# Optimization experiments

Measured on AMD Instinct MI355X. Metric: run time of the kernel, lower is better.

## Reference

```python
import jax, jax.numpy as jnp
import numpy as np

SHADOW_OFFSET = -1000.0
EPS_SIGMA = 1e-05
SIGMA_DIV = 2.1


def setup_inputs() -> dict:
    key = jax.random.key(0)
    k1, k2, k3, k4, k5, k6 = jax.random.split(key, 6)
    B, N, M, K, Kp, Din, Dout = 2, 65536, 16384, 32, 15, 64, 128
    points_xyz = jax.random.normal(k1, (B, N, 3), dtype=jnp.float32)
    features = jax.random.normal(k2, (B, Din, N), dtype=jnp.float32)
    center_xyz = jax.random.normal(k3, (B, M, 3), dtype=jnp.float32)
    neighbor_indices = jax.random.randint(k4, (B, M, K), 0, N + 1, dtype=jnp.int64)
    # kernel points in unit ball, 'center' fixed at origin (stand-in for load_kernels)
    kp = jax.random.normal(k5, (Kp, 3), dtype=jnp.float32)
    kp = kp / (jnp.linalg.norm(kp, axis=-1, keepdims=True) + 1e-6) * jax.random.uniform(k6, (Kp, 1)) ** (1.0 / 3.0)
    kernel_points = kp.at[0].set(0.0)
    # kaiming_uniform(a=sqrt(5)) on [Kp, Din, Dout]: fan_in = Din*Dout per torch semantics
    fan_in = Din * Dout
    bound = jnp.sqrt(6.0 / ((1.0 + 5.0) * fan_in)) * jnp.sqrt(3.0) / jnp.sqrt(3.0)
    bound = float(np.sqrt(6.0 / (6.0 * fan_in)))
    weights = jax.random.uniform(jax.random.fold_in(key, 7), (Kp, Din, Dout), minval=-bound, maxval=bound, dtype=jnp.float32)
    return {"points_xyz": points_xyz, "features": features, "center_xyz": center_xyz,
            "neighbor_indices": neighbor_indices, "kernel_points": kernel_points, "weights": weights}


def reference(points_xyz, features, center_xyz, neighbor_indices, kernel_points, weights):
    B, N, _ = points_xyz.shape
    M, K = neighbor_indices.shape[1], neighbor_indices.shape[2]
    Din = features.shape[1]
    # [B,N,3+Din] point coords + features, plus shadow point at index N
    points = jnp.concatenate([points_xyz, jnp.swapaxes(features, 1, 2)], axis=-1)
    shadow = jnp.zeros((B, 1, 3 + Din), points.dtype).at[:, :, :3].set(SHADOW_OFFSET)
    points = jnp.concatenate([points, shadow], axis=1)  # [B,N+1,3+Din]
    idx = neighbor_indices.reshape(B, M * K)
    gathered = jnp.take_along_axis(points, idx[:, :, None], axis=1).reshape(B, M, K, 3 + Din)
    neighbors_xyz = gathered[..., :3] - center_xyz[:, :, None, :]   # [B,M,K,3]
    neighbors_feats = gathered[..., 3:]                              # [B,M,K,Din]
    dist = jnp.sqrt(jnp.sum(neighbors_xyz ** 2, axis=3))             # [B,M,K]
    m_dist = jnp.max(dist, axis=2, keepdims=True)                    # [B,M,1]
    # radius=None path: kernel points scaled per center by max neighbor distance
    kp = kernel_points[None, None, :, :] * m_dist[:, :, :, None]     # [B,M,Kp,3]
    diffs = neighbors_xyz[:, :, :, None, :] - kp[:, :, None, :, :]   # [B,M,K,Kp,3]
    sq_d = jnp.sum(diffs ** 2, axis=4)                               # [B,M,K,Kp]
    sigma = m_dist[..., None] / SIGMA_DIV + EPS_SIGMA                # [B,M,1,1]
    w = jnp.clip(1.0 - jnp.sqrt(sq_d) / sigma, 0.0)                  # [B,M,K,Kp]
    weighted = jnp.einsum('bmkp,bmkd->bmpd', w, neighbors_feats)     # [B,M,Kp,Din]
    out = jnp.einsum('bmpd,pdo->bmo', weighted, weights)             # [B,M,Dout]
    return jnp.swapaxes(out, 1, 2)                                   # [B,Dout,M]
```

## Files before the change

kernel.cpp:

```cpp
#include <hip/hip_runtime.h>
#include <hip/hip_bf16.h>
#include <stdint.h>

#define B_    2
#define N_    65536
#define M_    16384
#define K_    32
#define KP_   15
#define DIN_  64
#define DOUT_ 128
#define TM    16
#define WPITCH 968

typedef __bf16 bf16x8 __attribute__((ext_vector_type(8)));
typedef float  f32x4  __attribute__((ext_vector_type(4)));
typedef float  f32x2  __attribute__((ext_vector_type(2)));

__device__ inline unsigned short f2bf(float f) {
    union { float f; unsigned int i; } v; v.f = f;
    unsigned int x = v.i;
    return (unsigned short)((x + 0x7fffu + ((x >> 16) & 1u)) >> 16);
}

__global__ __launch_bounds__(256) void transpose_feats(const float* __restrict__ feats,
                                                       unsigned short* __restrict__ featT) {
    const int b  = blockIdx.y;
    const int n0 = blockIdx.x * 64;
    const int t  = threadIdx.x;
    if (n0 >= N_) {
        if (t < 32)
            ((unsigned int*)(featT + ((size_t)b * (N_ + 1) + N_) * DIN_))[t] = 0u;
        return;
    }
    __shared__ float tile[64][65];
    const int nl = t & 63, dl = t >> 6;
    #pragma unroll
    for (int i = 0; i < 16; ++i) {
        int d = dl + 4 * i;
        tile[d][nl] = feats[((size_t)b * DIN_ + d) * N_ + n0 + nl];
    }
    __syncthreads();
    const int d2 = (t & 31) * 2;
    const int nr = t >> 5;
    #pragma unroll
    for (int i = 0; i < 8; ++i) {
        int n = nr + 8 * i;
        unsigned int u = ((unsigned int)f2bf(tile[d2 + 1][n]) << 16) | f2bf(tile[d2][n]);
        ((unsigned int*)(featT + ((size_t)b * (N_ + 1) + n0 + n) * DIN_))[t & 31] = u;
    }
}

__global__ __launch_bounds__(256) void build_wtfrag(const float* __restrict__ w,
                                                    unsigned short* __restrict__ wf) {
    int q = blockIdx.x * 256 + threadIdx.x;
    if (q >= 15360) return;
    int otile = q / 1920, r = q % 1920;
    int ks = r >> 6, lane = r & 63;
    int o  = otile * 16 + (lane & 15);
    int kb = ks * 32 + (lane >> 4) * 8;
    unsigned int d[4];
    #pragma unroll
    for (int j = 0; j < 4; ++j) {
        unsigned short lo = f2bf(w[(size_t)(kb + 2 * j) * 128 + o]);
        unsigned short hi = f2bf(w[(size_t)(kb + 2 * j + 1) * 128 + o]);
        d[j] = ((unsigned int)hi << 16) | lo;
    }
    *(uint4*)(wf + (size_t)q * 8) = make_uint4(d[0], d[1], d[2], d[3]);
}

__global__ __launch_bounds__(512, 1) void kpconv_fused(
    const float* __restrict__ points_xyz,
    const float* __restrict__ center_xyz,
    const int*   __restrict__ nidx,
    const float* __restrict__ kpts,
    const unsigned short* __restrict__ featT,
    const unsigned short* __restrict__ wtFrag,
    float* __restrict__ out) {

    __shared__ __align__(16) unsigned int  fbuf[TM * 32 * 32];
    __shared__ __align__(16) float         wlds[TM * KP_ * 32];
    __shared__ __align__(16) unsigned short wgt[TM * WPITCH];

    const int t  = threadIdx.x;
    const int b  = blockIdx.y;
    const int m0 = blockIdx.x * TM;
    const size_t ibase = ((size_t)b * M_ + m0) * K_;

    uint4 v[8];
    const int part = t & 7, rbase = t >> 3;
    #pragma unroll
    for (int i = 0; i < 8; ++i) {
        int r = i * 64 + rbase;
        int n = nidx[ibase + r];
        v[i] = *(const uint4*)(featT + ((size_t)b * (N_ + 1) + n) * DIN_ + part * 8);
    }

    {
        const int m = t >> 5, k = t & 31;
        int n = nidx[ibase + t];
        float px, py, pz;
        if (n < N_) {
            const float* p = points_xyz + ((size_t)b * N_ + n) * 3;
            px = p[0]; py = p[1]; pz = p[2];
        } else {
            px = py = pz = -1000.0f;
        }
        const float* c = center_xyz + ((size_t)b * M_ + m0 + m) * 3;
        float dx = px - c[0], dy = py - c[1], dz = pz - c[2];
        float md = __builtin_amdgcn_sqrtf(dx * dx + dy * dy + dz * dz);
        #pragma unroll
        for (int s = 16; s > 0; s >>= 1)
            md = fmaxf(md, __shfl_xor(md, s));
        float rsig = __builtin_amdgcn_rcpf(md * (1.0f / 2.1f) + 1e-5f);
        #pragma unroll
        for (int p = 0; p < KP_; ++p) {
            float ex = dx - kpts[p * 3 + 0] * md;
            float ey = dy - kpts[p * 3 + 1] * md;
            float ez = dz - kpts[p * 3 + 2] * md;
            float wv = 1.0f - __builtin_amdgcn_sqrtf(ex * ex + ey * ey + ez * ez) * rsig;
            wlds[(m * KP_ + p) * 32 + k] = wv > 0.0f ? wv : 0.0f;
        }
    }

    #pragma unroll
    for (int i = 0; i < 8; ++i)
        ((uint4*)fbuf)[(i * 64 + rbase) * 8 + part] = v[i];
    __syncthreads();

    {
        const int m = t >> 5, d2 = t & 31;
        f32x2 acc[KP_];
        #pragma unroll
        for (int p = 0; p < KP_; ++p) acc[p] = (f32x2){0.f, 0.f};

        const unsigned int* fcol = &fbuf[(m * 32) * 32 + d2];
        const float* wbase = &wlds[m * KP_ * 32];

        #pragma unroll
        for (int k4 = 0; k4 < 8; ++k4) {
            f32x2 fv[4];
            #pragma unroll
            for (int j = 0; j < 4; ++j) {
                unsigned int u = fcol[(k4 * 4 + j) * 32];
                union { unsigned int i; float f; } lo, hi;
                lo.i = u << 16; hi.i = u & 0xffff0000u;
                fv[j] = (f32x2){lo.f, hi.f};
            }
            #pragma unroll
            for (int p = 0; p < KP_; ++p) {
                float4 w4 = *(const float4*)(wbase + p * 32 + k4 * 4);
                acc[p] += fv[0] * w4.x;
                acc[p] += fv[1] * w4.y;
                acc[p] += fv[2] * w4.z;
                acc[p] += fv[3] * w4.w;
            }
        }

        unsigned int* wrow = (unsigned int*)wgt;
        #pragma unroll
        for (int p = 0; p < KP_; ++p) {
            unsigned int u = ((unsigned int)f2bf(acc[p][1]) << 16) | f2bf(acc[p][0]);
            wrow[m * (WPITCH / 2) + p * 32 + d2] = u;
        }
    }
    __syncthreads();

    {
        const int w = t >> 6, lane = t & 63;
        const char* aBase = (const char*)wgt + (lane & 15) * (WPITCH * 2) + (lane >> 4) * 16;
        const unsigned short* bPtr = wtFrag + ((size_t)(w * 30) * 64 + lane) * 8;

        f32x4 dacc = {0.f, 0.f, 0.f, 0.f};
        bf16x8 b0 = *(const bf16x8*)(bPtr);
        bf16x8 b1 = *(const bf16x8*)(bPtr + 512);
        bf16x8 b2 = *(const bf16x8*)(bPtr + 1024);
        bf16x8 b3 = *(const bf16x8*)(bPtr + 1536);
        bf16x8 b4 = *(const bf16x8*)(bPtr + 2048);

        #define S2_STEP(BX, KS, LD)                                           \
            {                                                                 \
                bf16x8 a = *(const bf16x8*)(aBase + (KS) * 64);               \
                dacc = __builtin_amdgcn_mfma_f32_16x16x32_bf16(a, BX, dacc,   \
                                                               0, 0, 0);      \
                if ((LD) < 30) BX = *(const bf16x8*)(bPtr + (size_t)(LD) * 512); \
            }

        for (int mi = 0; mi < 6; ++mi) {
            int ks = mi * 5;
            S2_STEP(b0, ks + 0, ks + 5);
            S2_STEP(b1, ks + 1, ks + 6);
            S2_STEP(b2, ks + 2, ks + 7);
            S2_STEP(b3, ks + 3, ks + 8);
            S2_STEP(b4, ks + 4, ks + 9);
        }
        #undef S2_STEP

        const int o = w * 16 + (lane & 15);
        float* dst = out + ((size_t)b * DOUT_ + o) * M_ + m0 + (lane >> 4) * 4;
        *(f32x4*)dst = dacc;
    }
}

extern "C" void kernel_launch(void* const* d_in, const int* in_sizes, int n_in,
                              void* d_out, int out_size, void* d_ws, size_t ws_size,
                              hipStream_t stream) {
    const float* points_xyz = (const float*)d_in[0];
    const float* features   = (const float*)d_in[1];
    const float* center_xyz = (const float*)d_in[2];
    const int*   nidx       = (const int*)d_in[3];
    const float* kpts       = (const float*)d_in[4];
    const float* weights    = (const float*)d_in[5];
    float* out = (float*)d_out;

    unsigned short* featT  = (unsigned short*)d_ws;
    unsigned short* wtFrag = (unsigned short*)((char*)d_ws + 16777472);

    transpose_feats<<<dim3((N_ + 64) / 64, B_), 256, 0, stream>>>(features, featT);
    build_wtfrag<<<60, 256, 0, stream>>>(weights, wtFrag);
    kpconv_fused<<<dim3(M_ / TM, B_), 512, 0, stream>>>(points_xyz, center_xyz, nidx,
                                                        kpts, featT, wtFrag, out);
}
```

Baseline: 170.7 us.

## Split stage-1 into two half-tile passes to cut LDS and raise occupancy

The fused kernel now processes the 16 centers in two halves of 8, halving the fbuf and wlds shared buffers and raising launch bounds to 4 blocks per CU. The second half's feature gathers are issued before the first half's stage-1 compute so global loads overlap with FMAs, and the weight fragments are prefetched before the second half. Stage-1 work is redistributed so each wave handles one center with two kernel-point halves per 64 lanes. In exchange it adds an extra barrier round, holds the kernel-point weights in registers across the halves, and the tighter register cap may cause spills.

After: 249.9 us. 1.46x slower.

```diff
diff --git a/kernel.cpp b/kernel.cpp
--- a/kernel.cpp
+++ b/kernel.cpp
@@ -68,7 +68,7 @@
     *(uint4*)(wf + (size_t)q * 8) = make_uint4(d[0], d[1], d[2], d[3]);
 }
 
-__global__ __launch_bounds__(512, 1) void kpconv_fused(
+__global__ __launch_bounds__(512, 4) void kpconv_fused(
     const float* __restrict__ points_xyz,
     const float* __restrict__ center_xyz,
     const int*   __restrict__ nidx,
@@ -77,26 +77,32 @@
     const unsigned short* __restrict__ wtFrag,
     float* __restrict__ out) {
 
-    __shared__ __align__(16) unsigned int  fbuf[TM * 32 * 32];
-    __shared__ __align__(16) float         wlds[TM * KP_ * 32];
+    __shared__ __align__(16) unsigned int   fbuf[8 * 32 * 32];
+    __shared__ __align__(16) float          wlds[8 * 16 * 32];
     __shared__ __align__(16) unsigned short wgt[TM * WPITCH];
 
     const int t  = threadIdx.x;
     const int b  = blockIdx.y;
     const int m0 = blockIdx.x * TM;
     const size_t ibase = ((size_t)b * M_ + m0) * K_;
-
-    uint4 v[8];
+    const size_t fbase = (size_t)b * (N_ + 1);
+
     const int part = t & 7, rbase = t >> 3;
-    #pragma unroll
-    for (int i = 0; i < 8; ++i) {
-        int r = i * 64 + rbase;
-        int n = nidx[ibase + r];
-        v[i] = *(const uint4*)(featT + ((size_t)b * (N_ + 1) + n) * DIN_ + part * 8);
-    }
-
+
+    int nA[4], nB[4];
+    #pragma unroll
+    for (int i = 0; i < 4; ++i) {
+        nA[i] = nidx[ibase + i * 64 + rbase];
+        nB[i] = nidx[ibase + 256 + i * 64 + rbase];
+    }
+    uint4 vA[4];
+    #pragma unroll
+    for (int i = 0; i < 4; ++i)
+        vA[i] = *(const uint4*)(featT + (fbase + nA[i]) * DIN_ + part * 8);
+
+    const int mw = t >> 5, kk = t & 31;
+    float wv[KP_];
     {
-        const int m = t >> 5, k = t & 31;
         int n = nidx[ibase + t];
         float px, py, pz;
         if (n < N_) {
@@ -105,7 +111,7 @@
         } else {
             px = py = pz = -1000.0f;
         }
-        const float* c = center_xyz + ((size_t)b * M_ + m0 + m) * 3;
+        const float* c = center_xyz + ((size_t)b * M_ + m0 + mw) * 3;
         float dx = px - c[0], dy = py - c[1], dz = pz - c[2];
         float md = __builtin_amdgcn_sqrtf(dx * dx + dy * dy + dz * dz);
         #pragma unroll
@@ -117,24 +123,30 @@
             float ex = dx - kpts[p * 3 + 0] * md;
             float ey = dy - kpts[p * 3 + 1] * md;
             float ez = dz - kpts[p * 3 + 2] * md;
-            float wv = 1.0f - __builtin_amdgcn_sqrtf(ex * ex + ey * ey + ez * ez) * rsig;
-            wlds[(m * KP_ + p) * 32 + k] = wv > 0.0f ? wv : 0.0f;
-        }
-    }
-
-    #pragma unroll
-    for (int i = 0; i < 8; ++i)
-        ((uint4*)fbuf)[(i * 64 + rbase) * 8 + part] = v[i];
-    __syncthreads();
-
-    {
-        const int m = t >> 5, d2 = t & 31;
-        f32x2 acc[KP_];
-        #pragma unroll
-        for (int p = 0; p < KP_; ++p) acc[p] = (f32x2){0.f, 0.f};
-
-        const unsigned int* fcol = &fbuf[(m * 32) * 32 + d2];
-        const float* wbase = &wlds[m * KP_ * 32];
+            float w = 1.0f - __builtin_amdgcn_sqrtf(ex * ex + ey * ey + ez * ez) * rsig;
+            wv[p] = w > 0.0f ? w : 0.0f;
+        }
+        if (mw < 8) {
+            #pragma unroll
+            for (int p = 0; p < KP_; ++p)
+                wlds[(mw * 16 + p) * 32 + kk] = wv[p];
+        }
+    }
+
+    #pragma unroll
+    for (int i = 0; i < 4; ++i)
+        ((uint4*)fbuf)[(i * 64 + rbase) * 8 + part] = vA[i];
+    __syncthreads();
+
+    auto stage1 = [&](int m) {
+        const int l  = t & 63;
+        const int d2 = l & 31, ph = l >> 5;
+        f32x2 acc[8];
+        #pragma unroll
+        for (int pl = 0; pl < 8; ++pl) acc[pl] = (f32x2){0.f, 0.f};
+
+        const unsigned int* fcol  = &fbuf[((m & 7) * 32) * 32 + d2];
+        const float*        wbase = &wlds[((m & 7) * 16 + ph * 8) * 32];
 
         #pragma unroll
         for (int k4 = 0; k4 < 8; ++k4) {
@@ -147,35 +159,56 @@
                 fv[j] = (f32x2){lo.f, hi.f};
             }
             #pragma unroll
-            for (int p = 0; p < KP_; ++p) {
-                float4 w4 = *(const float4*)(wbase + p * 32 + k4 * 4);
-                acc[p] += fv[0] * w4.x;
-                acc[p] += fv[1] * w4.y;
-                acc[p] += fv[2] * w4.z;
-                acc[p] += fv[3] * w4.w;
-            }
-        }
-
+            for (int pl = 0; pl < 8; ++pl) {
+                float4 w4 = *(const float4*)(wbase + pl * 32 + k4 * 4);
+                acc[pl] += fv[0] * w4.x;
+                acc[pl] += fv[1] * w4.y;
+                acc[pl] += fv[2] * w4.z;
+                acc[pl] += fv[3] * w4.w;
+            }
+        }
         unsigned int* wrow = (unsigned int*)wgt;
         #pragma unroll
-        for (int p = 0; p < KP_; ++p) {
-            unsigned int u = ((unsigned int)f2bf(acc[p][1]) << 16) | f2bf(acc[p][0]);
-            wrow[m * (WPITCH / 2) + p * 32 + d2] = u;
-        }
-    }
+        for (int pl = 0; pl < 8; ++pl) {
+            int p = ph * 8 + pl;
+            if (p < KP_) {
+                unsigned int u = ((unsigned int)f2bf(acc[pl][1]) << 16) | f2bf(acc[pl][0]);
+                wrow[m * (WPITCH / 2) + p * 32 + d2] = u;
+            }
+        }
+    };
+
+    uint4 vB[4];
+    #pragma unroll
+    for (int i = 0; i < 4; ++i)
+        vB[i] = *(const uint4*)(featT + (fbase + nB[i]) * DIN_ + part * 8);
+    stage1(t >> 6);
+    __syncthreads();
+
+    if (mw >= 8) {
+        #pragma unroll
+        for (int p = 0; p < KP_; ++p)
+            wlds[((mw - 8) * 16 + p) * 32 + kk] = wv[p];
+    }
+    #pragma unroll
+    for (int i = 0; i < 4; ++i)
+        ((uint4*)fbuf)[(i * 64 + rbase) * 8 + part] = vB[i];
+    __syncthreads();
+
+    const int w = t >> 6, lane = t & 63;
+    const unsigned short* bPtr = wtFrag + ((size_t)(w * 30) * 64 + lane) * 8;
+    bf16x8 b0 = *(const bf16x8*)(bPtr);
+    bf16x8 b1 = *(const bf16x8*)(bPtr + 512);
+    bf16x8 b2 = *(const bf16x8*)(bPtr + 1024);
+    bf16x8 b3 = *(const bf16x8*)(bPtr + 1536);
+    bf16x8 b4 = *(const bf16x8*)(bPtr + 2048);
+
+    stage1(8 + (t >> 6));
     __syncthreads();
 
     {
-        const int w = t >> 6, lane = t & 63;
         const char* aBase = (const char*)wgt + (lane & 15) * (WPITCH * 2) + (lane >> 4) * 16;
-        const unsigned short* bPtr = wtFrag + ((size_t)(w * 30) * 64 + lane) * 8;
-
         f32x4 dacc = {0.f, 0.f, 0.f, 0.f};
-        bf16x8 b0 = *(const bf16x8*)(bPtr);
-        bf16x8 b1 = *(const bf16x8*)(bPtr + 512);
-        bf16x8 b2 = *(const bf16x8*)(bPtr + 1024);
-        bf16x8 b3 = *(const bf16x8*)(bPtr + 1536);
-        bf16x8 b4 = *(const bf16x8*)(bPtr + 2048);
 
         #define S2_STEP(BX, KS, LD)                                           \
             {                                                                 \
```
